# Optimization experiments

Hardware: AMD Instinct MI355X
Metric: run time of the kernel (lower is better)

Reference implementation:

```python
import jax, jax.numpy as jnp
import numpy as np

B, K, H, W = 16, 64, 28, 28
HID, OUT = 128, 128
FLAT = 64 * 4 * 4  # 28 -> (28-5)//2+1=12 -> (12-5)//2+1=4 after two 5x5 stride-2 VALID convs


def setup_inputs() -> dict:
    key = jax.random.key(0)
    ks = jax.random.split(key, 12)
    g = lambda k, shape, s=0.05: jax.random.normal(k, shape, dtype=jnp.float32) * s
    return {
        "x": jax.random.normal(ks[0], (B, K, H, W), dtype=jnp.float32),
        "conv1_w": g(ks[1], (32, 1, 5, 5)),
        "conv1_b": g(ks[2], (32,)),
        "conv2_w": g(ks[3], (64, 32, 5, 5)),
        "conv2_b": g(ks[4], (64,)),
        "fc_w": g(ks[5], (HID, FLAT)),
        "fc_b": g(ks[6], (HID,)),
        "coeffs": g(ks[7], (HID, OUT, 15), float(np.sqrt(2.0 / (HID + OUT)))),
        "eq_bias": g(ks[8], (OUT,)),
        "diag_bias": g(ks[9], (OUT,)),
        "out_w": g(ks[10], (1, OUT)),
        "out_b": g(ks[11], (1,)),
    }


def _conv(x, w, b, stride):
    y = jax.lax.conv_general_dilated(x, w, (stride, stride), 'VALID',
                                     dimension_numbers=('NCHW', 'OIHW', 'NCHW'))
    return y + b[None, :, None, None]


def _ops_2_to_2(P):
    # P: (B, D, m, m) -> (B, D, 15, m, m), Maron et al. basis, 'inf' normalization
    m = P.shape[-1]
    mf = jnp.asarray(m, P.dtype)
    I = jnp.eye(m, dtype=P.dtype)
    diag = jnp.diagonal(P, axis1=-2, axis2=-1)            # (B,D,m)
    sum_diag = diag.sum(-1, keepdims=True)                # (B,D,1)
    sum_rows = P.sum(-1)                                  # (B,D,m)
    sum_cols = P.sum(-2)                                  # (B,D,m)
    sum_all = P.sum((-2, -1))[..., None, None]            # (B,D,1,1)
    de = lambda v: v[..., None] * I                       # diag_embed
    bc = lambda v: jnp.broadcast_to(v, P.shape)
    op1 = de(diag)
    op2 = de(jnp.broadcast_to(sum_diag, diag.shape)) / mf
    op3 = de(sum_rows) / mf
    op4 = de(sum_cols) / mf
    op5 = de(jnp.broadcast_to(sum_all[..., 0], diag.shape)) / (mf * mf)
    op6 = bc(sum_cols[..., :, None]) / mf
    op7 = bc(sum_rows[..., :, None]) / mf
    op8 = bc(sum_cols[..., None, :]) / mf
    op9 = bc(sum_rows[..., None, :]) / mf
    op10 = P
    op11 = jnp.swapaxes(P, -1, -2)
    op12 = bc(diag[..., :, None])
    op13 = bc(diag[..., None, :])
    op14 = bc(sum_diag[..., None]) / mf
    op15 = bc(sum_all) / (mf * mf)
    return jnp.stack([op1, op2, op3, op4, op5, op6, op7, op8,
                      op9, op10, op11, op12, op13, op14, op15], axis=2)


def reference(x, conv1_w, conv1_b, conv2_w, conv2_b, fc_w, fc_b,
              coeffs, eq_bias, diag_bias, out_w, out_b):
    Bx, k, h, w = x.shape
    y = x.reshape(Bx * k, 1, h, w)
    y = jax.nn.relu(_conv(y, conv1_w, conv1_b, 2))
    y = jax.nn.relu(_conv(y, conv2_w, conv2_b, 2))
    y = y.reshape(Bx * k, -1) @ fc_w.T + fc_b              # (B*k, HID)
    feat = y.reshape(Bx, k, -1)                            # (B, k, D)
    P = jnp.einsum('bid,bjd->bdij', feat, feat)            # (B, D, k, k)
    ops = _ops_2_to_2(P)                                   # (B, D, 15, k, k)
    out = jnp.einsum('dsp,bdpij->bsij', coeffs, ops)       # (B, S, k, k)
    out = out + eq_bias[None, :, None, None]
    out = out + jnp.eye(k, dtype=out.dtype) * diag_bias[None, :, None, None]
    out = jax.nn.relu(out).mean((-2, -1))                  # (B, S)
    out = jax.nn.relu(out)                                 # dropout_prob=0 / eval: identity
    return out @ out_w.T + out_b                           # (B, 1)
```

## Files before the change

### kernel.cpp

```cpp
#include <hip/hip_runtime.h>


#define FS_IDX(r, d) (((r) << 7) + (((((d) >> 2) ^ (((r) >> 2) & 7))) << 2) + ((d) & 3))

__global__ __launch_bounds__(256) void k_prep(
        const float* __restrict__ coeffs, const float* __restrict__ fc_w,
        const float* __restrict__ w2,
        float* __restrict__ CaT,  float* __restrict__ CdgT, float* __restrict__ CdrT,
        float* __restrict__ CugT, float* __restrict__ CurT,
        float* __restrict__ CvgT, float* __restrict__ CvrT,
        float* __restrict__ CctT, float* __restrict__ CcAT,
        float* __restrict__ CwtT, float* __restrict__ CwAT,
        float* __restrict__ fcwT, float* __restrict__ w2R,
        float* __restrict__ dout) {
    int idx = blockIdx.x * 256 + threadIdx.x;
    if (idx < 16384) {
        int d = idx >> 7, s = idx & 127;
        const float* c = coeffs + idx * 15;
        const float im = 1.0f / 64.0f, im2 = 1.0f / 4096.0f;
        int t = s * 128 + d;
        CaT[t]  = c[9] + c[10];
        CdgT[t] = c[0];
        CdrT[t] = (c[2] + c[3]) * im;
        CurT[t] = (c[5] + c[6]) * im;
        CugT[t] = c[11];
        CvrT[t] = (c[7] + c[8]) * im;
        CvgT[t] = c[12];
        CctT[t] = c[1] * im;
        CcAT[t] = c[4] * im2;
        CwtT[t] = c[13] * im;
        CwAT[t] = c[14] * im2;
        if (idx < 16) dout[idx] = 0.0f;
    } else if (idx < 147456) {
        int e = idx - 16384;
        int s = e >> 10, k = e & 1023;
        fcwT[k * 128 + s] = fc_w[e];
    } else if (idx < 198656) {
        int e = idx - 147456;
        int ic = e & 31;
        int q = e >> 5;
        int kx = q % 5, q2 = q / 5, ky = q2 % 5, oc = q2 / 5;
        w2R[e] = w2[oc * 800 + ic * 25 + ky * 5 + kx];
    }
}

__global__ __launch_bounds__(256) void k_convfc(
        const float* __restrict__ x,  const float* __restrict__ w1,
        const float* __restrict__ b1, const float* __restrict__ w2R,
        const float* __restrict__ b2, const float* __restrict__ fcwT,
        const float* __restrict__ fc_b, float* __restrict__ feat) {
    __shared__ alignas(16) float xs[1568];
    __shared__ alignas(16) float w1s[800];
    __shared__ alignas(16) float c1T[144 * 36];
    __shared__ alignas(16) float ysh[2][1024];
    __shared__ alignas(16) float ps[8][2][128];
    int tid = threadIdx.x;
    int n0 = blockIdx.x * 2;

    {
        const float4* xsrc = (const float4*)(x + n0 * 784);
        float4* xdst = (float4*)xs;
        for (int i = tid; i < 392; i += 256) xdst[i] = xsrc[i];
        const float4* wsrc = (const float4*)w1;
        float4* wdst = (float4*)w1s;
        for (int i = tid; i < 200; i += 256) wdst[i] = wsrc[i];
    }
    __syncthreads();

    for (int img = 0; img < 2; ++img) {
        for (int task = tid; task < 384; task += 256) {
            int oy = task >> 5, oc = task & 31;
            const float* wp = w1s + oc * 25;
            float wr[25];
#pragma unroll
            for (int t = 0; t < 25; ++t) wr[t] = wp[t];
            float out[12];
            float bv = b1[oc];
#pragma unroll
            for (int ox = 0; ox < 12; ++ox) out[ox] = bv;
            const float* xb = xs + img * 784 + (oy * 2) * 28;
#pragma unroll
            for (int ky = 0; ky < 5; ++ky) {
                const float4* rp = (const float4*)(xb + ky * 28);
                float4 r0 = rp[0], r1 = rp[1], r2 = rp[2], r3 = rp[3];
                float4 r4 = rp[4], r5 = rp[5], r6 = rp[6];
                float rf[28] = {r0.x, r0.y, r0.z, r0.w, r1.x, r1.y, r1.z, r1.w,
                                r2.x, r2.y, r2.z, r2.w, r3.x, r3.y, r3.z, r3.w,
                                r4.x, r4.y, r4.z, r4.w, r5.x, r5.y, r5.z, r5.w,
                                r6.x, r6.y, r6.z, r6.w};
#pragma unroll
                for (int kx = 0; kx < 5; ++kx) {
                    float wv = wr[ky * 5 + kx];
#pragma unroll
                    for (int ox = 0; ox < 12; ++ox)
                        out[ox] = fmaf(rf[2 * ox + kx], wv, out[ox]);
                }
            }
#pragma unroll
            for (int ox = 0; ox < 12; ++ox)
                c1T[(oy * 12 + ox) * 36 + oc] = fmaxf(out[ox], 0.0f);
        }
        __syncthreads();

        {
            int icg = tid & 3, oc = tid >> 2;
            int ic0 = icg * 8;
            float acc[16];
#pragma unroll
            for (int p = 0; p < 16; ++p) acc[p] = 0.0f;
            for (int ky = 0; ky < 5; ++ky) {
                float4 wv[5][2];
#pragma unroll
                for (int kx = 0; kx < 5; ++kx) {
                    const float* wb = &w2R[((oc * 5 + ky) * 5 + kx) * 32 + ic0];
                    wv[kx][0] = *(const float4*)(wb);
                    wv[kx][1] = *(const float4*)(wb + 4);
                }
#pragma unroll
                for (int oyy = 0; oyy < 4; ++oyy) {
                    int y = 2 * oyy + ky;
                    const float* rowb = c1T + (y * 12) * 36 + ic0;
#pragma unroll
                    for (int xx = 0; xx < 12; ++xx) {
                        float4 v0 = *(const float4*)(rowb + xx * 36);
                        float4 v1 = *(const float4*)(rowb + xx * 36 + 4);
#pragma unroll
                        for (int ox = 0; ox < 4; ++ox) {
                            int kx = xx - 2 * ox;
                            if (kx >= 0 && kx < 5) {
                                float4 w0 = wv[kx][0], w1v = wv[kx][1];
                                float s = acc[oyy * 4 + ox];
                                s = fmaf(v0.x, w0.x, s);
                                s = fmaf(v0.y, w0.y, s);
                                s = fmaf(v0.z, w0.z, s);
                                s = fmaf(v0.w, w0.w, s);
                                s = fmaf(v1.x, w1v.x, s);
                                s = fmaf(v1.y, w1v.y, s);
                                s = fmaf(v1.z, w1v.z, s);
                                s = fmaf(v1.w, w1v.w, s);
                                acc[oyy * 4 + ox] = s;
                            }
                        }
                    }
                }
            }
#pragma unroll
            for (int m = 1; m < 4; m <<= 1)
#pragma unroll
                for (int p = 0; p < 16; ++p)
                    acc[p] += __shfl_xor(acc[p], m);
            if (icg == 0) {
                float bb = b2[oc];
#pragma unroll
                for (int p = 0; p < 16; ++p)
                    ysh[img][oc * 16 + p] = fmaxf(acc[p] + bb, 0.0f);
            }
        }
        __syncthreads();
    }

    {
        int sg = tid & 31, kc = tid >> 5;
        const float* yb0 = &ysh[0][kc * 128];
        const float* yb1 = &ysh[1][kc * 128];
        const float* wb = fcwT + kc * 128 * 128 + sg * 4;
        float4 a0 = {0.f, 0.f, 0.f, 0.f}, a1 = {0.f, 0.f, 0.f, 0.f};
#pragma unroll 4
        for (int i = 0; i < 128; ++i) {
            float4 w = *(const float4*)(wb + i * 128);
            float y0 = yb0[i], y1 = yb1[i];
            a0.x = fmaf(y0, w.x, a0.x); a0.y = fmaf(y0, w.y, a0.y);
            a0.z = fmaf(y0, w.z, a0.z); a0.w = fmaf(y0, w.w, a0.w);
            a1.x = fmaf(y1, w.x, a1.x); a1.y = fmaf(y1, w.y, a1.y);
            a1.z = fmaf(y1, w.z, a1.z); a1.w = fmaf(y1, w.w, a1.w);
        }
        *(float4*)&ps[kc][0][sg * 4] = a0;
        *(float4*)&ps[kc][1][sg * 4] = a1;
    }
    __syncthreads();
    {
        int img = tid >> 7, s = tid & 127;
        float acc = fc_b[s];
#pragma unroll
        for (int kc = 0; kc < 8; ++kc) acc += ps[kc][img][s];
        feat[(n0 + img) * 128 + s] = acc;
    }
}

__global__ __launch_bounds__(256) void k_main2(
        const float* __restrict__ feat,
        const float* __restrict__ CaT,  const float* __restrict__ CdgT,
        const float* __restrict__ CdrT, const float* __restrict__ CugT,
        const float* __restrict__ CurT, const float* __restrict__ CvgT,
        const float* __restrict__ CvrT, const float* __restrict__ CctT,
        const float* __restrict__ CcAT, const float* __restrict__ CwtT,
        const float* __restrict__ CwAT,
        const float* __restrict__ eq_bias, const float* __restrict__ diag_bias,
        const float* __restrict__ out_w,   const float* __restrict__ out_b,
        float* __restrict__ dout) {
    __shared__ alignas(16) float fs[8192];
    __shared__ alignas(16) float ash2[512];
    __shared__ alignas(16) float Ssh[128];
    __shared__ float Uv[4][64], Vv[4][64], Dv[4][64];
    __shared__ float parts[2][8];
    __shared__ float red[4][4];
    int b = blockIdx.x >> 5, sq = blockIdx.x & 31;
    int s0 = sq * 4;
    int tid = threadIdx.x;
    const float* fb = feat + b * 8192;

    for (int i = tid; i < 8192; i += 256) {
        int r = i >> 7, d = i & 127;
        fs[FS_IDX(r, d)] = fb[i];
    }
    for (int i = tid; i < 512; i += 256) {
        int d = i >> 2, sl = i & 3;
        ash2[d * 4 + sl] = CaT[(s0 + sl) * 128 + d];
    }
    __syncthreads();

    if (tid < 128) {
        int d = tid;
        float sv = 0.f, tv = 0.f;
        for (int r = 0; r < 64; ++r) {
            float v = fs[FS_IDX(r, d)];
            sv += v;
            tv = fmaf(v, v, tv);
        }
        Ssh[d] = sv;
        float av = sv * sv;
        float dc[4], wv[4];
#pragma unroll
        for (int sl = 0; sl < 4; ++sl) {
            int o = (s0 + sl) * 128 + d;
            dc[sl] = fmaf(CctT[o], tv, CcAT[o] * av);
            wv[sl] = fmaf(CwtT[o], tv, CwAT[o] * av);
        }
#pragma unroll
        for (int m = 1; m < 64; m <<= 1)
#pragma unroll
            for (int sl = 0; sl < 4; ++sl) {
                dc[sl] += __shfl_xor(dc[sl], m);
                wv[sl] += __shfl_xor(wv[sl], m);
            }
        if ((tid & 63) == 0) {
            int w = tid >> 6;
#pragma unroll
            for (int sl = 0; sl < 4; ++sl) {
                parts[w][sl] = dc[sl];
                parts[w][4 + sl] = wv[sl];
            }
        }
    }
    __syncthreads();

    int tx = tid & 15, ty = tid >> 4;
    {
        int d0 = tx * 8;
        float4 s0v = *(const float4*)&Ssh[d0];
        float4 s1v = *(const float4*)&Ssh[d0 + 4];
        float sv[8] = {s0v.x, s0v.y, s0v.z, s0v.w, s1v.x, s1v.y, s1v.z, s1v.w};
#pragma unroll
        for (int sl = 0; sl < 4; ++sl) {
            int o = (s0 + sl) * 128 + d0;
            float4 A0, A1;
#define LD8(arr, p) A0 = *(const float4*)&arr[o]; A1 = *(const float4*)&arr[o + 4]; \
            float p[8] = {A0.x, A0.y, A0.z, A0.w, A1.x, A1.y, A1.z, A1.w};
            LD8(CdgT, cg) LD8(CdrT, cr) LD8(CugT, ug) LD8(CurT, ur) LD8(CvgT, vg) LD8(CvrT, vr)
#undef LD8
            float pD[4], pU[4], pV[4];
#pragma unroll
            for (int u = 0; u < 4; ++u) {
                int i = ty * 4 + u;
                float4 fA = *(const float4*)&fs[FS_IDX(i, d0)];
                float4 fB = *(const float4*)&fs[FS_IDX(i, d0 + 4)];
                float fv[8] = {fA.x, fA.y, fA.z, fA.w, fB.x, fB.y, fB.z, fB.w};
                float aD = 0.f, aU = 0.f, aV = 0.f;
#pragma unroll
                for (int e = 0; e < 8; ++e) {
                    float g = fv[e] * fv[e];
                    float rr = fv[e] * sv[e];
                    aD = fmaf(cg[e], g, fmaf(cr[e], rr, aD));
                    aU = fmaf(ug[e], g, fmaf(ur[e], rr, aU));
                    aV = fmaf(vg[e], g, fmaf(vr[e], rr, aV));
                }
                pD[u] = aD; pU[u] = aU; pV[u] = aV;
            }
#pragma unroll
            for (int m = 1; m < 16; m <<= 1)
#pragma unroll
                for (int u = 0; u < 4; ++u) {
                    pD[u] += __shfl_xor(pD[u], m);
                    pU[u] += __shfl_xor(pU[u], m);
                    pV[u] += __shfl_xor(pV[u], m);
                }
            if (tx == 0)
#pragma unroll
                for (int u = 0; u < 4; ++u) {
                    Dv[sl][ty * 4 + u] = pD[u];
                    Uv[sl][ty * 4 + u] = pU[u];
                    Vv[sl][ty * 4 + u] = pV[u];
                }
        }
    }
    __syncthreads();

    float acc[4][16];
#pragma unroll
    for (int sl = 0; sl < 4; ++sl)
#pragma unroll
        for (int q = 0; q < 16; ++q) acc[sl][q] = 0.f;
    for (int d = 0; d < 128; d += 4) {
        float aif[4][4], bjf[4][4], a4f[4][4];
#pragma unroll
        for (int u = 0; u < 4; ++u) {
            float4 t = *(const float4*)&fs[FS_IDX(ty * 4 + u, d)];
            aif[u][0] = t.x; aif[u][1] = t.y; aif[u][2] = t.z; aif[u][3] = t.w;
        }
#pragma unroll
        for (int v = 0; v < 4; ++v) {
            float4 t = *(const float4*)&fs[FS_IDX(tx * 4 + v, d)];
            bjf[v][0] = t.x; bjf[v][1] = t.y; bjf[v][2] = t.z; bjf[v][3] = t.w;
        }
#pragma unroll
        for (int dd = 0; dd < 4; ++dd) {
            float4 t = *(const float4*)&ash2[(d + dd) * 4];
            a4f[dd][0] = t.x; a4f[dd][1] = t.y; a4f[dd][2] = t.z; a4f[dd][3] = t.w;
        }
#pragma unroll
        for (int dd = 0; dd < 4; ++dd)
#pragma unroll
            for (int sl = 0; sl < 4; ++sl)
#pragma unroll
                for (int u = 0; u < 4; ++u) {
                    float t = aif[u][dd] * a4f[dd][sl];
#pragma unroll
                    for (int v = 0; v < 4; ++v)
                        acc[sl][u * 4 + v] = fmaf(t, bjf[v][dd], acc[sl][u * 4 + v]);
                }
    }

    float sDc[4], sW[4];
#pragma unroll
    for (int sl = 0; sl < 4; ++sl) {
        sDc[sl] = parts[0][sl] + parts[1][sl] + diag_bias[s0 + sl];
        sW[sl]  = parts[0][4 + sl] + parts[1][4 + sl] + eq_bias[s0 + sl];
    }
    float psum[4] = {0.f, 0.f, 0.f, 0.f};
#pragma unroll
    for (int u = 0; u < 4; ++u) {
        int i = ty * 4 + u;
#pragma unroll
        for (int v = 0; v < 4; ++v) {
            int j = tx * 4 + v;
#pragma unroll
            for (int sl = 0; sl < 4; ++sl) {
                float val = acc[sl][u * 4 + v] + Uv[sl][i] + Vv[sl][j] + sW[sl];
                if (i == j) val += Dv[sl][i] + sDc[sl];
                psum[sl] += fmaxf(val, 0.0f);
            }
        }
    }
#pragma unroll
    for (int m = 1; m < 64; m <<= 1)
#pragma unroll
        for (int sl = 0; sl < 4; ++sl) psum[sl] += __shfl_xor(psum[sl], m);
    if ((tid & 63) == 0) {
        int w = tid >> 6;
#pragma unroll
        for (int sl = 0; sl < 4; ++sl) red[w][sl] = psum[sl];
    }
    __syncthreads();
    if (tid == 0) {
        float o = 0.f;
#pragma unroll
        for (int sl = 0; sl < 4; ++sl) {
            float tot = red[0][sl] + red[1][sl] + red[2][sl] + red[3][sl];
            o += fmaxf(tot * (1.0f / 4096.0f), 0.0f) * out_w[s0 + sl];
        }
        if (s0 == 0) o += out_b[0];
        atomicAdd(dout + b, o);
    }
}

extern "C" void kernel_launch(void* const* d_in, const int* in_sizes, int n_in,
                              void* d_out, int out_size, void* d_ws, size_t ws_size,
                              hipStream_t stream) {
    const float* x      = (const float*)d_in[0];
    const float* w1     = (const float*)d_in[1];
    const float* b1     = (const float*)d_in[2];
    const float* w2     = (const float*)d_in[3];
    const float* b2     = (const float*)d_in[4];
    const float* fc_w   = (const float*)d_in[5];
    const float* fc_b   = (const float*)d_in[6];
    const float* coeffs = (const float*)d_in[7];
    const float* eqb    = (const float*)d_in[8];
    const float* dgb    = (const float*)d_in[9];
    const float* out_w  = (const float*)d_in[10];
    const float* out_b  = (const float*)d_in[11];

    float* ws = (float*)d_ws;
    float* feat = ws; ws += 131072;
    float* fcwT = ws; ws += 131072;
    float* w2R  = ws; ws += 51200;
    float* CaT  = ws; ws += 16384;
    float* CdgT = ws; ws += 16384;
    float* CdrT = ws; ws += 16384;
    float* CugT = ws; ws += 16384;
    float* CurT = ws; ws += 16384;
    float* CvgT = ws; ws += 16384;
    float* CvrT = ws; ws += 16384;
    float* CctT = ws; ws += 16384;
    float* CcAT = ws; ws += 16384;
    float* CwtT = ws; ws += 16384;
    float* CwAT = ws; ws += 16384;

    k_prep<<<776, 256, 0, stream>>>(coeffs, fc_w, w2,
                                    CaT, CdgT, CdrT, CugT, CurT, CvgT, CvrT,
                                    CctT, CcAT, CwtT, CwAT, fcwT, w2R,
                                    (float*)d_out);
    k_convfc<<<512, 256, 0, stream>>>(x, w1, b1, w2R, b2, fcwT, fc_b, feat);
    k_main2<<<512, 256, 0, stream>>>(feat, CaT, CdgT, CdrT, CugT, CurT,
                                     CvgT, CvrT, CctT, CcAT, CwtT, CwAT,
                                     eqb, dgb, out_w, out_b, (float*)d_out);
}
```

Before: 173.4 us.

## Double grid parallelism for conv/FC and main kernels, replace atomics with final reduction

```diff
diff --git a/kernel.cpp b/kernel.cpp
--- a/kernel.cpp
+++ b/kernel.cpp
@@ -11,8 +11,7 @@
         float* __restrict__ CvgT, float* __restrict__ CvrT,
         float* __restrict__ CctT, float* __restrict__ CcAT,
         float* __restrict__ CwtT, float* __restrict__ CwAT,
-        float* __restrict__ fcwT, float* __restrict__ w2R,
-        float* __restrict__ dout) {
+        float* __restrict__ fcwT, float* __restrict__ w2R) {
     int idx = blockIdx.x * 256 + threadIdx.x;
     if (idx < 16384) {
         int d = idx >> 7, s = idx & 127;
@@ -30,7 +29,6 @@
         CcAT[t] = c[4] * im2;
         CwtT[t] = c[13] * im;
         CwAT[t] = c[14] * im2;
-        if (idx < 16) dout[idx] = 0.0f;
     } else if (idx < 147456) {
         int e = idx - 16384;
         int s = e >> 10, k = e & 1023;
@@ -49,141 +47,134 @@
         const float* __restrict__ b1, const float* __restrict__ w2R,
         const float* __restrict__ b2, const float* __restrict__ fcwT,
         const float* __restrict__ fc_b, float* __restrict__ feat) {
-    __shared__ alignas(16) float xs[1568];
+    __shared__ alignas(16) float xs[784];
     __shared__ alignas(16) float w1s[800];
     __shared__ alignas(16) float c1T[144 * 36];
-    __shared__ alignas(16) float ysh[2][1024];
-    __shared__ alignas(16) float ps[8][2][128];
+    __shared__ alignas(16) float ysh[1024];
+    __shared__ alignas(16) float ps[8][128];
     int tid = threadIdx.x;
-    int n0 = blockIdx.x * 2;
+    int n = blockIdx.x;
 
     {
-        const float4* xsrc = (const float4*)(x + n0 * 784);
+        const float4* xsrc = (const float4*)(x + n * 784);
         float4* xdst = (float4*)xs;
-        for (int i = tid; i < 392; i += 256) xdst[i] = xsrc[i];
+        for (int i = tid; i < 196; i += 256) xdst[i] = xsrc[i];
         const float4* wsrc = (const float4*)w1;
         float4* wdst = (float4*)w1s;
         for (int i = tid; i < 200; i += 256) wdst[i] = wsrc[i];
     }
     __syncthreads();
 
-    for (int img = 0; img < 2; ++img) {
-        for (int task = tid; task < 384; task += 256) {
-            int oy = task >> 5, oc = task & 31;
-            const float* wp = w1s + oc * 25;
-            float wr[25];
-#pragma unroll
-            for (int t = 0; t < 25; ++t) wr[t] = wp[t];
-            float out[12];
-            float bv = b1[oc];
-#pragma unroll
-            for (int ox = 0; ox < 12; ++ox) out[ox] = bv;
-            const float* xb = xs + img * 784 + (oy * 2) * 28;
-#pragma unroll
-            for (int ky = 0; ky < 5; ++ky) {
-                const float4* rp = (const float4*)(xb + ky * 28);
-                float4 r0 = rp[0], r1 = rp[1], r2 = rp[2], r3 = rp[3];
-                float4 r4 = rp[4], r5 = rp[5], r6 = rp[6];
-                float rf[28] = {r0.x, r0.y, r0.z, r0.w, r1.x, r1.y, r1.z, r1.w,
-                                r2.x, r2.y, r2.z, r2.w, r3.x, r3.y, r3.z, r3.w,
-                                r4.x, r4.y, r4.z, r4.w, r5.x, r5.y, r5.z, r5.w,
-                                r6.x, r6.y, r6.z, r6.w};
-#pragma unroll
-                for (int kx = 0; kx < 5; ++kx) {
-                    float wv = wr[ky * 5 + kx];
-#pragma unroll
-                    for (int ox = 0; ox < 12; ++ox)
-                        out[ox] = fmaf(rf[2 * ox + kx], wv, out[ox]);
-                }
-            }
-#pragma unroll
-            for (int ox = 0; ox < 12; ++ox)
-                c1T[(oy * 12 + ox) * 36 + oc] = fmaxf(out[ox], 0.0f);
-        }
-        __syncthreads();
-
-        {
-            int icg = tid & 3, oc = tid >> 2;
-            int ic0 = icg * 8;
-            float acc[16];
-#pragma unroll
-            for (int p = 0; p < 16; ++p) acc[p] = 0.0f;
-            for (int ky = 0; ky < 5; ++ky) {
-                float4 wv[5][2];
-#pragma unroll
-                for (int kx = 0; kx < 5; ++kx) {
-                    const float* wb = &w2R[((oc * 5 + ky) * 5 + kx) * 32 + ic0];
-                    wv[kx][0] = *(const float4*)(wb);
-                    wv[kx][1] = *(const float4*)(wb + 4);
-                }
-#pragma unroll
-                for (int oyy = 0; oyy < 4; ++oyy) {
-                    int y = 2 * oyy + ky;
-                    const float* rowb = c1T + (y * 12) * 36 + ic0;
-#pragma unroll
-                    for (int xx = 0; xx < 12; ++xx) {
-                        float4 v0 = *(const float4*)(rowb + xx * 36);
-                        float4 v1 = *(const float4*)(rowb + xx * 36 + 4);
-#pragma unroll
-                        for (int ox = 0; ox < 4; ++ox) {
-                            int kx = xx - 2 * ox;
-                            if (kx >= 0 && kx < 5) {
-                                float4 w0 = wv[kx][0], w1v = wv[kx][1];
-                                float s = acc[oyy * 4 + ox];
-                                s = fmaf(v0.x, w0.x, s);
-                                s = fmaf(v0.y, w0.y, s);
-                                s = fmaf(v0.z, w0.z, s);
-                                s = fmaf(v0.w, w0.w, s);
-                                s = fmaf(v1.x, w1v.x, s);
-                                s = fmaf(v1.y, w1v.y, s);
-                                s = fmaf(v1.z, w1v.z, s);
-                                s = fmaf(v1.w, w1v.w, s);
-                                acc[oyy * 4 + ox] = s;
-                            }
+#pragma unroll
+    for (int rep = 0; rep < 3; ++rep) {
+        int task = rep * 256 + tid;
+        int oc = task & 31, oh = (task >> 5) & 1, oy = task >> 6;
+        const float* wp = w1s + oc * 25;
+        float wr[25];
+#pragma unroll
+        for (int t = 0; t < 25; ++t) wr[t] = wp[t];
+        float out[6];
+        float bv = b1[oc];
+#pragma unroll
+        for (int ox = 0; ox < 6; ++ox) out[ox] = bv;
+        const float* xb = xs + (oy * 2) * 28 + oh * 12;
+#pragma unroll
+        for (int ky = 0; ky < 5; ++ky) {
+            const float4* rp = (const float4*)(xb + ky * 28 - oh * 12) + 3 * oh;
+            float4 r0 = rp[0], r1 = rp[1], r2 = rp[2], r3 = rp[3];
+            float rf[16] = {r0.x, r0.y, r0.z, r0.w, r1.x, r1.y, r1.z, r1.w,
+                            r2.x, r2.y, r2.z, r2.w, r3.x, r3.y, r3.z, r3.w};
+#pragma unroll
+            for (int kx = 0; kx < 5; ++kx) {
+                float wv = wr[ky * 5 + kx];
+#pragma unroll
+                for (int ox = 0; ox < 6; ++ox)
+                    out[ox] = fmaf(rf[2 * ox + kx], wv, out[ox]);
+            }
+        }
+#pragma unroll
+        for (int ox = 0; ox < 6; ++ox)
+            c1T[(oy * 12 + oh * 6 + ox) * 36 + oc] = fmaxf(out[ox], 0.0f);
+    }
+    __syncthreads();
+
+    {
+        int icg = tid & 3, oc = tid >> 2;
+        int ic0 = icg * 8;
+        float acc[16];
+#pragma unroll
+        for (int p = 0; p < 16; ++p) acc[p] = 0.0f;
+        for (int ky = 0; ky < 5; ++ky) {
+            float4 wv[5][2];
+#pragma unroll
+            for (int kx = 0; kx < 5; ++kx) {
+                const float* wb = &w2R[((oc * 5 + ky) * 5 + kx) * 32 + ic0];
+                wv[kx][0] = *(const float4*)(wb);
+                wv[kx][1] = *(const float4*)(wb + 4);
+            }
+#pragma unroll
+            for (int oyy = 0; oyy < 4; ++oyy) {
+                int y = 2 * oyy + ky;
+                const float* rowb = c1T + (y * 12) * 36 + ic0;
+#pragma unroll
+                for (int xx = 0; xx < 12; ++xx) {
+                    float4 v0 = *(const float4*)(rowb + xx * 36);
+                    float4 v1 = *(const float4*)(rowb + xx * 36 + 4);
+#pragma unroll
+                    for (int ox = 0; ox < 4; ++ox) {
+                        int kx = xx - 2 * ox;
+                        if (kx >= 0 && kx < 5) {
+                            float4 w0 = wv[kx][0], w1v = wv[kx][1];
+                            float s = acc[oyy * 4 + ox];
+                            s = fmaf(v0.x, w0.x, s);
+                            s = fmaf(v0.y, w0.y, s);
+                            s = fmaf(v0.z, w0.z, s);
+                            s = fmaf(v0.w, w0.w, s);
+                            s = fmaf(v1.x, w1v.x, s);
+                            s = fmaf(v1.y, w1v.y, s);
+                            s = fmaf(v1.z, w1v.z, s);
+                            s = fmaf(v1.w, w1v.w, s);
+                            acc[oyy * 4 + ox] = s;
                         }
                     }
                 }
             }
-#pragma unroll
-            for (int m = 1; m < 4; m <<= 1)
-#pragma unroll
-                for (int p = 0; p < 16; ++p)
-                    acc[p] += __shfl_xor(acc[p], m);
-            if (icg == 0) {
-                float bb = b2[oc];
-#pragma unroll
-                for (int p = 0; p < 16; ++p)
-                    ysh[img][oc * 16 + p] = fmaxf(acc[p] + bb, 0.0f);
-            }
-        }
-        __syncthreads();
-    }
+        }
+#pragma unroll
+        for (int m = 1; m < 4; m <<= 1)
+#pragma unroll
+            for (int p = 0; p < 16; ++p)
+                acc[p] += __shfl_xor(acc[p], m);
+        if (icg == 0) {
+            float bb = b2[oc];
+#pragma unroll
+            for (int p = 0; p < 16; ++p)
+                ysh[oc * 16 + p] = fmaxf(acc[p] + bb, 0.0f);
+        }
+    }
+    __syncthreads();
 
     {
         int sg = tid & 31, kc = tid >> 5;
-        const float* yb0 = &ysh[0][kc * 128];
-        const float* yb1 = &ysh[1][kc * 128];
+        const float* yb = &ysh[kc * 128];
         const float* wb = fcwT + kc * 128 * 128 + sg * 4;
-        float4 a0 = {0.f, 0.f, 0.f, 0.f}, a1 = {0.f, 0.f, 0.f, 0.f};
+        float4 a0 = {0.f, 0.f, 0.f, 0.f};
 #pragma unroll 4
         for (int i = 0; i < 128; ++i) {
             float4 w = *(const float4*)(wb + i * 128);
-            float y0 = yb0[i], y1 = yb1[i];
+            float y0 = yb[i];
             a0.x = fmaf(y0, w.x, a0.x); a0.y = fmaf(y0, w.y, a0.y);
             a0.z = fmaf(y0, w.z, a0.z); a0.w = fmaf(y0, w.w, a0.w);
-            a1.x = fmaf(y1, w.x, a1.x); a1.y = fmaf(y1, w.y, a1.y);
-            a1.z = fmaf(y1, w.z, a1.z); a1.w = fmaf(y1, w.w, a1.w);
-        }
-        *(float4*)&ps[kc][0][sg * 4] = a0;
-        *(float4*)&ps[kc][1][sg * 4] = a1;
-    }
-    __syncthreads();
-    {
-        int img = tid >> 7, s = tid & 127;
+        }
+        *(float4*)&ps[kc][sg * 4] = a0;
+    }
+    __syncthreads();
+    if (tid < 128) {
+        int s = tid;
         float acc = fc_b[s];
 #pragma unroll
-        for (int kc = 0; kc < 8; ++kc) acc += ps[kc][img][s];
-        feat[(n0 + img) * 128 + s] = acc;
+        for (int kc = 0; kc < 8; ++kc) acc += ps[kc][s];
+        feat[n * 128 + s] = acc;
     }
 }
 
@@ -196,16 +187,16 @@
         const float* __restrict__ CcAT, const float* __restrict__ CwtT,
         const float* __restrict__ CwAT,
         const float* __restrict__ eq_bias, const float* __restrict__ diag_bias,
-        const float* __restrict__ out_w,   const float* __restrict__ out_b,
-        float* __restrict__ dout) {
+        const float* __restrict__ out_w,
+        float* __restrict__ partials) {
     __shared__ alignas(16) float fs[8192];
-    __shared__ alignas(16) float ash2[512];
+    __shared__ alignas(16) float ash2[256];
     __shared__ alignas(16) float Ssh[128];
-    __shared__ float Uv[4][64], Vv[4][64], Dv[4][64];
-    __shared__ float parts[2][8];
-    __shared__ float red[4][4];
-    int b = blockIdx.x >> 5, sq = blockIdx.x & 31;
-    int s0 = sq * 4;
+    __shared__ float Uv[2][64], Vv[2][64], Dv[2][64];
+    __shared__ float parts[2][4];
+    __shared__ float red[4][2];
+    int b = blockIdx.x >> 6, sq = blockIdx.x & 63;
+    int s0 = sq * 2;
     int tid = threadIdx.x;
     const float* fb = feat + b * 8192;
 
@@ -213,9 +204,9 @@
         int r = i >> 7, d = i & 127;
         fs[FS_IDX(r, d)] = fb[i];
     }
-    for (int i = tid; i < 512; i += 256) {
-        int d = i >> 2, sl = i & 3;
-        ash2[d * 4 + sl] = CaT[(s0 + sl) * 128 + d];
+    if (tid < 256) {
+        int d = tid >> 1, sl = tid & 1;
+        ash2[d * 2 + sl] = CaT[(s0 + sl) * 128 + d];
     }
     __syncthreads();
 
@@ -229,9 +220,9 @@
         }
         Ssh[d] = sv;
         float av = sv * sv;
-        float dc[4], wv[4];
-#pragma unroll
-        for (int sl = 0; sl < 4; ++sl) {
+        float dc[2], wv[2];
+#pragma unroll
+        for (int sl = 0; sl < 2; ++sl) {
             int o = (s0 + sl) * 128 + d;
             dc[sl] = fmaf(CctT[o], tv, CcAT[o] * av);
             wv[sl] = fmaf(CwtT[o], tv, CwAT[o] * av);
@@ -239,16 +230,16 @@
 #pragma unroll
         for (int m = 1; m < 64; m <<= 1)
 #pragma unroll
-            for (int sl = 0; sl < 4; ++sl) {
+            for (int sl = 0; sl < 2; ++sl) {
                 dc[sl] += __shfl_xor(dc[sl], m);
                 wv[sl] += __shfl_xor(wv[sl], m);
             }
         if ((tid & 63) == 0) {
             int w = tid >> 6;
 #pragma unroll
-            for (int sl = 0; sl < 4; ++sl) {
+            for (int sl = 0; sl < 2; ++sl) {
                 parts[w][sl] = dc[sl];
-                parts[w][4 + sl] = wv[sl];
+                parts[w][2 + sl] = wv[sl];
             }
         }
     }
@@ -261,7 +252,7 @@
         float4 s1v = *(const float4*)&Ssh[d0 + 4];
         float sv[8] = {s0v.x, s0v.y, s0v.z, s0v.w, s1v.x, s1v.y, s1v.z, s1v.w};
 #pragma unroll
-        for (int sl = 0; sl < 4; ++sl) {
+        for (int sl = 0; sl < 2; ++sl) {
             int o = (s0 + sl) * 128 + d0;
             float4 A0, A1;
 #define LD8(arr, p) A0 = *(const float4*)&arr[o]; A1 = *(const float4*)&arr[o + 4]; \
@@ -305,13 +296,13 @@
     }
     __syncthreads();
 
-    float acc[4][16];
-#pragma unroll
-    for (int sl = 0; sl < 4; ++sl)
+    float acc[2][16];
+#pragma unroll
+    for (int sl = 0; sl < 2; ++sl)
 #pragma unroll
         for (int q = 0; q < 16; ++q) acc[sl][q] = 0.f;
     for (int d = 0; d < 128; d += 4) {
-        float aif[4][4], bjf[4][4], a4f[4][4];
+        float aif[4][4], bjf[4][4], a4f[4][2];
 #pragma unroll
         for (int u = 0; u < 4; ++u) {
             float4 t = *(const float4*)&fs[FS_IDX(ty * 4 + u, d)];
@@ -323,14 +314,15 @@
             bjf[v][0] = t.x; bjf[v][1] = t.y; bjf[v][2] = t.z; bjf[v][3] = t.w;
         }
 #pragma unroll
-        for (int dd = 0; dd < 4; ++dd) {
-            float4 t = *(const float4*)&ash2[(d + dd) * 4];
-            a4f[dd][0] = t.x; a4f[dd][1] = t.y; a4f[dd][2] = t.z; a4f[dd][3] = t.w;
+        for (int dd = 0; dd < 2; ++dd) {
+            float4 t = *(const float4*)&ash2[(d + dd * 2) * 2];
+            a4f[dd * 2][0] = t.x;     a4f[dd * 2][1] = t.y;
+            a4f[dd * 2 + 1][0] = t.z; a4f[dd * 2 + 1][1] = t.w;
         }
 #pragma unroll
         for (int dd = 0; dd < 4; ++dd)
 #pragma unroll
-            for (int sl = 0; sl < 4; ++sl)
+            for (int sl = 0; sl < 2; ++sl)
 #pragma unroll
                 for (int u = 0; u < 4; ++u) {
                     float t = aif[u][dd] * a4f[dd][sl];
@@ -340,13 +332,13 @@
                 }
     }
 
-    float sDc[4], sW[4];
-#pragma unroll
-    for (int sl = 0; sl < 4; ++sl) {
+    float sDc[2], sW[2];
+#pragma unroll
+    for (int sl = 0; sl < 2; ++sl) {
         sDc[sl] = parts[0][sl] + parts[1][sl] + diag_bias[s0 + sl];
-        sW[sl]  = parts[0][4 + sl] + parts[1][4 + sl] + eq_bias[s0 + sl];
-    }
-    float psum[4] = {0.f, 0.f, 0.f, 0.f};
+        sW[sl]  = parts[0][2 + sl] + parts[1][2 + sl] + eq_bias[s0 + sl];
+    }
+    float psum[2] = {0.f, 0.f};
 #pragma unroll
     for (int u = 0; u < 4; ++u) {
         int i = ty * 4 + u;
@@ -354,7 +346,7 @@
         for (int v = 0; v < 4; ++v) {
             int j = tx * 4 + v;
 #pragma unroll
-            for (int sl = 0; sl < 4; ++sl) {
+            for (int sl = 0; sl < 2; ++sl) {
                 float val = acc[sl][u * 4 + v] + Uv[sl][i] + Vv[sl][j] + sW[sl];
                 if (i == j) val += Dv[sl][i] + sDc[sl];
                 psum[sl] += fmaxf(val, 0.0f);
@@ -364,23 +356,32 @@
 #pragma unroll
     for (int m = 1; m < 64; m <<= 1)
 #pragma unroll
-        for (int sl = 0; sl < 4; ++sl) psum[sl] += __shfl_xor(psum[sl], m);
+        for (int sl = 0; sl < 2; ++sl) psum[sl] += __shfl_xor(psum[sl], m);
     if ((tid & 63) == 0) {
         int w = tid >> 6;
 #pragma unroll
-        for (int sl = 0; sl < 4; ++sl) red[w][sl] = psum[sl];
+        for (int sl = 0; sl < 2; ++sl) red[w][sl] = psum[sl];
     }
     __syncthreads();
     if (tid == 0) {
         float o = 0.f;
 #pragma unroll
-        for (int sl = 0; sl < 4; ++sl) {
+        for (int sl = 0; sl < 2; ++sl) {
             float tot = red[0][sl] + red[1][sl] + red[2][sl] + red[3][sl];
             o += fmaxf(tot * (1.0f / 4096.0f), 0.0f) * out_w[s0 + sl];
         }
-        if (s0 == 0) o += out_b[0];
-        atomicAdd(dout + b, o);
-    }
+        partials[blockIdx.x] = o;
+    }
+}
+
+__global__ __launch_bounds__(64) void k_final(
+        const float* __restrict__ partials, const float* __restrict__ out_b,
+        float* __restrict__ dout) {
+    int b = blockIdx.x, lane = threadIdx.x;
+    float v = partials[b * 64 + lane];
+#pragma unroll
+    for (int m = 1; m < 64; m <<= 1) v += __shfl_xor(v, m);
+    if (lane == 0) dout[b] = v + out_b[0];
 }
 
 extern "C" void kernel_launch(void* const* d_in, const int* in_sizes, int n_in,
@@ -403,6 +404,7 @@
     float* feat = ws; ws += 131072;
     float* fcwT = ws; ws += 131072;
     float* w2R  = ws; ws += 51200;
+    float* prt  = ws; ws += 1024;
     float* CaT  = ws; ws += 16384;
     float* CdgT = ws; ws += 16384;
     float* CdrT = ws; ws += 16384;
@@ -417,10 +419,10 @@
 
     k_prep<<<776, 256, 0, stream>>>(coeffs, fc_w, w2,
                                     CaT, CdgT, CdrT, CugT, CurT, CvgT, CvrT,
-                                    CctT, CcAT, CwtT, CwAT, fcwT, w2R,
-                                    (float*)d_out);
-    k_convfc<<<512, 256, 0, stream>>>(x, w1, b1, w2R, b2, fcwT, fc_b, feat);
-    k_main2<<<512, 256, 0, stream>>>(feat, CaT, CdgT, CdrT, CugT, CurT,
-                                     CvgT, CvrT, CctT, CcAT, CwtT, CwAT,
-                                     eqb, dgb, out_w, out_b, (float*)d_out);
+                                    CctT, CcAT, CwtT, CwAT, fcwT, w2R);
+    k_convfc<<<1024, 256, 0, stream>>>(x, w1, b1, w2R, b2, fcwT, fc_b, feat);
+    k_main2<<<1024, 256, 0, stream>>>(feat, CaT, CdgT, CdrT, CugT, CurT,
+                                      CvgT, CvrT, CctT, CcAT, CwtT, CwAT,
+                                      eqb, dgb, out_w, prt);
+    k_final<<<16, 64, 0, stream>>>(prt, out_b, (float*)d_out);
 }
```

After: 173.7 us. About the same (+0.2%).
